# Kernel tuning notes

Measured on AMD Instinct MI355X. Metric: run time of the kernel, lower is better.

The kernel has to match this reference:

```python
import jax, jax.numpy as jnp
import numpy as np

B = 16384
D1 = 256
D2 = 256
D_FF = 1024
N_BINS = 16
TAIL = 3.0
MIN_VAL = 1e-3
MIN_TOTAL = N_BINS * MIN_VAL
TAIL_CONST = float(np.log(np.exp(1.0 - MIN_VAL) - 1.0))
D_OUT = (3 * N_BINS - 1) * D2  # 12032


def setup_inputs() -> dict:
    key = jax.random.key(0)
    ks = jax.random.split(key, 8)
    s = lambda fan: 1.0 / np.sqrt(fan)
    return {
        'x1': jax.random.normal(ks[0], (B, D1), jnp.float32),
        'x2': jax.random.normal(ks[1], (B, D2), jnp.float32),
        'W0': jax.random.normal(ks[2], (D1, D_FF), jnp.float32) * s(D1),
        'b0': jnp.zeros((D_FF,), jnp.float32),
        'W1': jax.random.normal(ks[3], (D_FF, D_FF), jnp.float32) * s(D_FF),
        'b1': jnp.zeros((D_FF,), jnp.float32),
        'W2': jax.random.normal(ks[4], (D_FF, D_OUT), jnp.float32) * s(D_FF),
        'b2': jnp.zeros((D_OUT,), jnp.float32),
    }


def _rqs_forward(x, wu, hu, du):
    # x: [B, D2]; wu, hu: [B, D2, N_BINS]; du: [B, D2, N_BINS-1]
    widths = MIN_VAL + (1.0 - MIN_TOTAL) * jax.nn.softmax(wu, axis=-1)
    heights = MIN_VAL + (1.0 - MIN_TOTAL) * jax.nn.softmax(hu, axis=-1)
    cw = jnp.cumsum(widths, axis=-1)
    cw = jnp.concatenate([jnp.zeros_like(cw[..., :1]), cw], axis=-1)
    cw = 2.0 * TAIL * cw - TAIL  # x bin edges in [-TAIL, TAIL], [B,D2,N_BINS+1]
    ch = jnp.cumsum(heights, axis=-1)
    ch = jnp.concatenate([jnp.zeros_like(ch[..., :1]), ch], axis=-1)
    ch = 2.0 * TAIL * ch - TAIL  # y bin edges
    w = cw[..., 1:] - cw[..., :-1]
    h = ch[..., 1:] - ch[..., :-1]
    # boundary derivatives padded so softplus(TAIL_CONST)+MIN_VAL == 1 (linear tails)
    pad = jnp.full_like(du[..., :1], TAIL_CONST)
    d = MIN_VAL + jax.nn.softplus(jnp.concatenate([pad, du, pad], axis=-1))  # [B,D2,N_BINS+1]
    inside = (x > -TAIL) & (x < TAIL)
    xc = jnp.clip(x, -TAIL, TAIL)
    # data-dependent bin search against interior edges
    idx = jnp.sum((xc[..., None] >= cw[..., 1:-1]).astype(jnp.int32), axis=-1)  # [B,D2]
    take = lambda a: jnp.take_along_axis(a, idx[..., None], axis=-1)[..., 0]
    xk = take(cw[..., :-1]); yk = take(ch[..., :-1])
    wk = take(w); hk = take(h)
    dk = take(d[..., :-1]); dk1 = take(d[..., 1:])
    sk = hk / wk
    theta = (xc - xk) / wk
    t1m = theta * (1.0 - theta)
    denom = sk + (dk + dk1 - 2.0 * sk) * t1m
    y = yk + hk * (sk * theta * theta + dk * t1m) / denom
    deriv = sk * sk * (dk1 * theta * theta + 2.0 * sk * t1m + dk * (1.0 - theta) ** 2) / (denom * denom)
    y = jnp.where(inside, y, x)            # identity tails
    logdet = jnp.where(inside, jnp.log(deriv), 0.0)
    return y, jnp.sum(logdet, axis=-1)     # [B,D2], [B]


def reference(x1, x2, W0, b0, W1, b1, W2, b2):
    # conditioner MLP: x1 -> spline parameters
    hdn = jax.nn.relu(x1 @ W0 + b0)
    hdn = jax.nn.relu(hdn @ W1 + b1)
    p = (hdn @ W2 + b2).reshape(-1, D2, 3 * N_BINS - 1)
    wu = p[..., :N_BINS]
    hu = p[..., N_BINS:2 * N_BINS]
    du = p[..., 2 * N_BINS:]
    y2, logdet = _rqs_forward(x2, wu, hu, du)
    return y2, logdet
```

## Files before the change

kernel.cpp:

```cpp
#include <hip/hip_runtime.h>
#include <math.h>

using u16 = unsigned short;
using bf16x8 = __attribute__((ext_vector_type(8))) short;
using f32x4  = __attribute__((ext_vector_type(4))) float;

#define DEV static __device__ __forceinline__

DEV u16 f2bf(float f) {
  union { float f; unsigned u; } v; v.f = f;
  unsigned u = v.u + 0x7fffu + ((v.u >> 16) & 1u);
  return (u16)(u >> 16);
}

DEV void gload16(const void* g, void* l) {
  __builtin_amdgcn_global_load_lds(
      (const __attribute__((address_space(1))) void*)g,
      (__attribute__((address_space(3))) void*)l, 16, 0, 0);
}

__global__ void k_conv_bf16(const float* __restrict__ in, u16* __restrict__ out, int n) {
  int i = blockIdx.x * 256 + threadIdx.x;
  if (i < n) out[i] = f2bf(in[i]);
}

__global__ void k_transconv(const float* __restrict__ in, u16* __restrict__ out,
                            int K, int Nin, int Nout, int pack) {
  __shared__ float t[32][33];
  int kb = blockIdx.x * 32, nb = blockIdx.y * 32;
  int tx = threadIdx.x & 31, ty = threadIdx.x >> 5;
  #pragma unroll
  for (int i = 0; i < 4; ++i) {
    int k = kb + ty + i * 8;
    int no = nb + tx;
    float v = 0.f;
    if (k < K && no < Nout) {
      if (pack) {
        int r = no % 48;
        if (r < 47) v = in[(size_t)k * Nin + (no / 48) * 47 + r];
      } else {
        v = in[(size_t)k * Nin + no];
      }
    }
    t[ty + i * 8][tx] = v;
  }
  __syncthreads();
  #pragma unroll
  for (int i = 0; i < 4; ++i) {
    int no = nb + ty + i * 8;
    int k = kb + tx;
    if (no < Nout && k < K) out[(size_t)no * K + k] = f2bf(t[tx][ty + i * 8]);
  }
}

__global__ __launch_bounds__(256)
void k_gemm_relu(const u16* __restrict__ A, const u16* __restrict__ Bt,
                 const float* __restrict__ bias, u16* __restrict__ C,
                 int N, int K) {
  constexpr int BM = 128, BN = 128, BK = 32;
  __shared__ __align__(16) u16 lds[(BM + BN) * BK];
  int tid = threadIdx.x, w = tid >> 6, lane = tid & 63;
  int bn = blockIdx.x, bm = blockIdx.y;
  int brow = bm * BM, bcol = bn * BN;
  int wm = w >> 1, wn = w & 1;
  int fr = lane & 15, fg = lane >> 4;
  f32x4 acc[4][4];
  #pragma unroll
  for (int i = 0; i < 4; ++i)
    #pragma unroll
    for (int j = 0; j < 4; ++j) acc[i][j] = (f32x4){0.f, 0.f, 0.f, 0.f};

  constexpr int ACH = BM * BK / 8;
  constexpr int CALLS = (BM + BN) * BK / 8 / 64;

  for (int kt = 0; kt < K; kt += BK) {
    for (int j = 0; j * 4 + w < CALLS; ++j) {
      int cb = (j * 4 + w) * 64;
      int c = cb + lane;
      const u16* g;
      if (c < ACH) {
        int row = c >> 2, c8 = c & 3;
        g = A + (size_t)(brow + row) * K + kt + c8 * 8;
      } else {
        int b = c - ACH;
        int nn = b >> 2, c8 = b & 3;
        g = Bt + (size_t)(bcol + nn) * K + kt + c8 * 8;
      }
      gload16(g, &lds[cb * 8]);
    }
    asm volatile("s_waitcnt vmcnt(0)" ::: "memory");
    __syncthreads();

    const u16* Al = lds;
    const u16* Bl = lds + BM * BK;
    bf16x8 af[4], bfr[4];
    #pragma unroll
    for (int mi = 0; mi < 4; ++mi)
      af[mi] = *(const bf16x8*)&Al[(wm * 64 + mi * 16 + fr) * BK + fg * 8];
    #pragma unroll
    for (int ni = 0; ni < 4; ++ni)
      bfr[ni] = *(const bf16x8*)&Bl[(wn * 64 + ni * 16 + fr) * BK + fg * 8];
    #pragma unroll
    for (int mi = 0; mi < 4; ++mi)
      #pragma unroll
      for (int ni = 0; ni < 4; ++ni)
        acc[mi][ni] = __builtin_amdgcn_mfma_f32_16x16x32_bf16(af[mi], bfr[ni], acc[mi][ni], 0, 0, 0);
    __syncthreads();
  }

  #pragma unroll
  for (int ni = 0; ni < 4; ++ni) {
    int col = bcol + wn * 64 + ni * 16 + fr;
    float bb = bias[col];
    #pragma unroll
    for (int mi = 0; mi < 4; ++mi) {
      #pragma unroll
      for (int q = 0; q < 4; ++q) {
        int row = brow + wm * 64 + mi * 16 + fg * 4 + q;
        float vv = acc[mi][ni][q] + bb;
        C[(size_t)row * N + col] = f2bf(vv > 0.f ? vv : 0.f);
      }
    }
  }
}

__global__ __launch_bounds__(256, 2)
void k_gemm3_fused(const u16* __restrict__ A, const u16* __restrict__ Bt,
                   const float* __restrict__ b2, const float* __restrict__ x2,
                   float* __restrict__ y2, float* __restrict__ ldpart) {
  extern __shared__ char smem[];
  const int tid = threadIdx.x, w = tid >> 6, lane = tid & 63;
  const int wm = w >> 1, wn = w & 1;
  const int fr = lane & 15, fg = lane >> 4;

  const int bid = blockIdx.x;
  const int bm = bid >> 6;
  const int bn = ((bid & 7) << 3) | ((bid >> 3) & 7);
  const int brow = bm * 128;

  const int csrc = (tid & 3) ^ ((tid >> 3) & 3);
  const u16* gA0 = A + (size_t)(brow + (tid >> 2)) * 1024 + csrc * 8;
  const u16* gB0 = Bt + (size_t)(bn * 192 + (tid >> 2)) * 1024 + csrc * 8;

#define STAGE(t1, sb) {                                               \
    const size_t ko_ = (size_t)(t1) * 32;                             \
    char* p_ = smem + (sb) + tid * 16;                                \
    gload16(gA0 + ko_, p_);                                           \
    gload16(gA0 + 65536 + ko_, p_ + 4096);                            \
    gload16(gB0 + ko_, p_ + 8192);                                    \
    gload16(gB0 + 65536 + ko_, p_ + 12288);                           \
    gload16(gB0 + 131072 + ko_, p_ + 16384); }

  const int sc = ((fg ^ ((fr >> 1) & 3)) << 4);

  f32x4 acc[4][6];
  #pragma unroll
  for (int m = 0; m < 4; ++m)
    #pragma unroll
    for (int n = 0; n < 6; ++n) acc[m][n] = (f32x4){0.f, 0.f, 0.f, 0.f};

#define COMPUTE(sb) {                                                 \
    const char* Ab_ = smem + (sb);                                    \
    const char* Bb_ = Ab_ + 8192;                                     \
    bf16x8 b_[6];                                                     \
    _Pragma("unroll")                                                 \
    for (int n_ = 0; n_ < 6; ++n_)                                    \
      b_[n_] = *(const bf16x8*)(Bb_ + (wn * 96 + n_ * 16 + fr) * 64 + sc); \
    __builtin_amdgcn_s_setprio(1);                                    \
    _Pragma("unroll")                                                 \
    for (int m_ = 0; m_ < 4; ++m_) {                                  \
      bf16x8 a_ = *(const bf16x8*)(Ab_ + (wm * 64 + m_ * 16 + fr) * 64 + sc); \
      _Pragma("unroll")                                               \
      for (int n_ = 0; n_ < 6; ++n_)                                  \
        acc[m_][n_] = __builtin_amdgcn_mfma_f32_16x16x32_bf16(a_, b_[n_], acc[m_][n_], 0, 0, 0); \
    }                                                                 \
    __builtin_amdgcn_s_setprio(0); }

#define VMW(n) { asm volatile("s_waitcnt vmcnt(" #n ")" ::: "memory"); \
                 __builtin_amdgcn_sched_barrier(0); }
#define RBAR() { __builtin_amdgcn_s_barrier(); __builtin_amdgcn_sched_barrier(0); }

  STAGE(0, 0); STAGE(1, 20480);
  VMW(5);
  RBAR();

  for (int j = 0; j < 10; ++j) {
    STAGE(3 * j + 2, 40960); COMPUTE(0);     VMW(5); RBAR();
    STAGE(3 * j + 3, 0);     COMPUTE(20480); VMW(5); RBAR();
    STAGE(3 * j + 4, 20480); COMPUTE(40960); VMW(5); RBAR();
  }
  COMPUTE(0); VMW(0); RBAR();
  COMPUTE(20480);
  __syncthreads();

  float* ldacc = (float*)(smem + 50176);
  float* fl = (float*)smem;
  #pragma unroll
  for (int rh = 0; rh < 2; ++rh) {
    if (wm == rh) {
      #pragma unroll
      for (int m = 0; m < 4; ++m)
        #pragma unroll
        for (int n = 0; n < 6; ++n) {
          const int g = wn * 2 + (n >= 3 ? 1 : 0);
          const int ci = (n % 3) * 16 + fr;
          #pragma unroll
          for (int q = 0; q < 4; ++q)
            fl[g * 3136 + (m * 16 + fg * 4 + q) * 49 + ci] = acc[m][n][q];
        }
    }
    __syncthreads();
    {
      const int g = tid >> 6, r = tid & 63;
      const float* pr = fl + g * 3136 + r * 49;
      const int grow = brow + rh * 64 + r;
      const int d2 = bn * 4 + g;
      const float* bb = b2 + (size_t)d2 * 47;

      float wv[16], hv[16];
      #pragma unroll
      for (int j = 0; j < 16; ++j) wv[j] = pr[j] + bb[j];
      #pragma unroll
      for (int j = 0; j < 16; ++j) hv[j] = pr[16 + j] + bb[16 + j];

      float x = x2[(size_t)grow * 256 + d2];
      float xc = fminf(fmaxf(x, -3.f), 3.f);

      float mw = wv[0];
      #pragma unroll
      for (int j = 1; j < 16; ++j) mw = fmaxf(mw, wv[j]);
      float sw = 0.f;
      #pragma unroll
      for (int j = 0; j < 16; ++j) { wv[j] = __expf(wv[j] - mw); sw += wv[j]; }
      float scw = 0.984f / sw;

      float mh = hv[0];
      #pragma unroll
      for (int j = 1; j < 16; ++j) mh = fmaxf(mh, hv[j]);
      float sh = 0.f;
      #pragma unroll
      for (int j = 0; j < 16; ++j) { hv[j] = __expf(hv[j] - mh); sh += hv[j]; }
      float sch = 0.984f / sh;

      int idx = 0;
      float xk = -3.f, cum = 0.f;
      #pragma unroll
      for (int i = 1; i <= 15; ++i) {
        cum += 0.001f + wv[i - 1] * scw;
        float cwi = 6.f * cum - 3.f;
        if (xc >= cwi) { idx = i; xk = cwi; }
      }
      float yk = -3.f, cumh = 0.f;
      #pragma unroll
      for (int i = 1; i <= 15; ++i) {
        cumh += 0.001f + hv[i - 1] * sch;
        float chi = 6.f * cumh - 3.f;
        if (i == idx) yk = chi;
      }
      float wk = 1.f, hk = 1.f;
      #pragma unroll
      for (int i = 0; i < 16; ++i) {
        if (i == idx) {
          wk = 6.f * (0.001f + wv[i] * scw);
          hk = 6.f * (0.001f + hv[i] * sch);
        }
      }
      float dk = 1.f, dk1 = 1.f;
      #pragma unroll
      for (int i = 1; i <= 15; ++i) {
        float u = pr[32 + i - 1] + bb[32 + i - 1];
        float e = __expf(u);
        float dd = 0.001f + (u > 15.f ? u : log1pf(e));
        if (i == idx) dk = dd;
        if (i == idx + 1) dk1 = dd;
      }

      float sk = hk / wk;
      float th = (xc - xk) / wk;
      float om = 1.f - th;
      float t1m = th * om;
      float den = sk + (dk + dk1 - 2.f * sk) * t1m;
      float y = yk + hk * (sk * th * th + dk * t1m) / den;
      float deriv = sk * sk * (dk1 * th * th + 2.f * sk * t1m + dk * om * om) / (den * den);
      bool inside = (x > -3.f) && (x < 3.f);
      float yout = inside ? y : x;
      float ld = inside ? __logf(deriv) : 0.f;

      y2[(size_t)grow * 256 + d2] = yout;
      ldacc[(rh * 64 + r) * 4 + g] = ld;
    }
    __syncthreads();
  }

  if (tid < 128) {
    float s = ldacc[tid * 4] + ldacc[tid * 4 + 1] + ldacc[tid * 4 + 2] + ldacc[tid * 4 + 3];
    ldpart[(size_t)bn * 16384 + brow + tid] = s;
  }
}

__global__ void k_reduce_ld(const float* __restrict__ part, float* __restrict__ out) {
  int r = blockIdx.x * 256 + threadIdx.x;
  float s = 0.f;
  for (int j = 0; j < 64; ++j) s += part[(size_t)j * 16384 + r];
  out[r] = s;
}

extern "C" void kernel_launch(void* const* d_in, const int* in_sizes, int n_in,
                              void* d_out, int out_size, void* d_ws, size_t ws_size,
                              hipStream_t stream) {
  const float* x1 = (const float*)d_in[0];
  const float* x2 = (const float*)d_in[1];
  const float* W0 = (const float*)d_in[2];
  const float* b0 = (const float*)d_in[3];
  const float* W1 = (const float*)d_in[4];
  const float* b1 = (const float*)d_in[5];
  const float* W2 = (const float*)d_in[6];
  const float* b2 = (const float*)d_in[7];
  float* y2 = (float*)d_out;
  float* logdet = y2 + (size_t)16384 * 256;

  char* ws = (char*)d_ws;
  u16* W2t = (u16*)ws;
  u16* W0t = (u16*)(ws + 25165824);
  u16* W1t = (u16*)(ws + 25165824 + 524288);
  u16* x1b = (u16*)(ws + 27787264);
  float* ldp = (float*)(ws + 27787264);
  u16* h1  = (u16*)(ws + 36175872);
  u16* h2  = (u16*)(ws + 69730304);

  hipFuncSetAttribute((const void*)k_gemm3_fused,
                      hipFuncAttributeMaxDynamicSharedMemorySize, 61440);

  k_conv_bf16<<<16384, 256, 0, stream>>>(x1, x1b, 16384 * 256);
  k_transconv<<<dim3(8, 32), 256, 0, stream>>>(W0, W0t, 256, 1024, 1024, 0);
  k_transconv<<<dim3(32, 32), 256, 0, stream>>>(W1, W1t, 1024, 1024, 1024, 0);
  k_transconv<<<dim3(32, 384), 256, 0, stream>>>(W2, W2t, 1024, 12032, 12288, 1);

  k_gemm_relu<<<dim3(8, 128), 256, 0, stream>>>(x1b, W0t, b0, h1, 1024, 256);
  k_gemm_relu<<<dim3(8, 128), 256, 0, stream>>>(h1, W1t, b1, h2, 1024, 1024);
  k_gemm3_fused<<<8192, 256, 61440, stream>>>(h2, W2t, b2, x2, y2, ldp);
  k_reduce_ld<<<64, 256, 0, stream>>>(ldp, logdet);
}
```

Measured before the change: 708.6 us.

## Pre-pack GEMM3 operands into tile-contiguous swizzled layout for contiguous loads

The second hidden GEMM and the W2 transpose-convert kernel now write their outputs in a blocked layout. Each 128-row (or 192-row) by 32-k tile is stored contiguously with the LDS XOR swizzle already applied. The fused GEMM3 then streams each stage as fully contiguous 16-byte chunks, with no strided per-row addressing. The aim is better global load coalescing and fewer TLB/row misses, at the cost of scattered 2-byte writes in the producer epilogues.

New measurement: 725.6 us. 1.02x slower.

```diff
diff --git a/kernel.cpp b/kernel.cpp
--- a/kernel.cpp
+++ b/kernel.cpp
@@ -49,14 +49,24 @@
   for (int i = 0; i < 4; ++i) {
     int no = nb + ty + i * 8;
     int k = kb + tx;
-    if (no < Nout && k < K) out[(size_t)no * K + k] = f2bf(t[tx][ty + i * 8]);
+    if (no < Nout && k < K) {
+      float v = t[tx][ty + i * 8];
+      if (pack) {
+        int r_ = no % 192, bn_ = no / 192;
+        int t_ = k >> 5, c_ = k & 31;
+        out[(((size_t)bn_ * 32 + t_) * 192 + r_) * 32
+            + (((c_ >> 3) ^ ((r_ >> 1) & 3)) << 3) + (c_ & 7)] = f2bf(v);
+      } else {
+        out[(size_t)no * K + k] = f2bf(v);
+      }
+    }
   }
 }
 
 __global__ __launch_bounds__(256)
 void k_gemm_relu(const u16* __restrict__ A, const u16* __restrict__ Bt,
                  const float* __restrict__ bias, u16* __restrict__ C,
-                 int N, int K) {
+                 int N, int K, int pack) {
   constexpr int BM = 128, BN = 128, BK = 32;
   __shared__ __align__(16) u16 lds[(BM + BN) * BK];
   int tid = threadIdx.x, w = tid >> 6, lane = tid & 63;
@@ -118,14 +128,21 @@
       for (int q = 0; q < 4; ++q) {
         int row = brow + wm * 64 + mi * 16 + fg * 4 + q;
         float vv = acc[mi][ni][q] + bb;
-        C[(size_t)row * N + col] = f2bf(vv > 0.f ? vv : 0.f);
+        u16 ov = f2bf(vv > 0.f ? vv : 0.f);
+        if (pack) {
+          int t_ = col >> 5, c_ = col & 31, r_ = row & 127;
+          C[(((size_t)(row >> 7) * 32 + t_) * 128 + r_) * 32
+            + (((c_ >> 3) ^ ((r_ >> 1) & 3)) << 3) + (c_ & 7)] = ov;
+        } else {
+          C[(size_t)row * N + col] = ov;
+        }
       }
     }
   }
 }
 
 __global__ __launch_bounds__(256, 2)
-void k_gemm3_fused(const u16* __restrict__ A, const u16* __restrict__ Bt,
+void k_gemm3_fused(const u16* __restrict__ Apack, const u16* __restrict__ Bpack,
                    const float* __restrict__ b2, const float* __restrict__ x2,
                    float* __restrict__ y2, float* __restrict__ ldpart) {
   extern __shared__ char smem[];
@@ -138,18 +155,18 @@
   const int bn = ((bid & 7) << 3) | ((bid >> 3) & 7);
   const int brow = bm * 128;
 
-  const int csrc = (tid & 3) ^ ((tid >> 3) & 3);
-  const u16* gA0 = A + (size_t)(brow + (tid >> 2)) * 1024 + csrc * 8;
-  const u16* gB0 = Bt + (size_t)(bn * 192 + (tid >> 2)) * 1024 + csrc * 8;
+  const u16* gA0 = Apack + (size_t)bm * 131072 + tid * 8;
+  const u16* gB0 = Bpack + (size_t)bn * 196608 + tid * 8;
 
 #define STAGE(t1, sb) {                                               \
-    const size_t ko_ = (size_t)(t1) * 32;                             \
+    const u16* pa_ = gA0 + (size_t)(t1) * 4096;                       \
+    const u16* pb_ = gB0 + (size_t)(t1) * 6144;                       \
     char* p_ = smem + (sb) + tid * 16;                                \
-    gload16(gA0 + ko_, p_);                                           \
-    gload16(gA0 + 65536 + ko_, p_ + 4096);                            \
-    gload16(gB0 + ko_, p_ + 8192);                                    \
-    gload16(gB0 + 65536 + ko_, p_ + 12288);                           \
-    gload16(gB0 + 131072 + ko_, p_ + 16384); }
+    gload16(pa_, p_);                                                 \
+    gload16(pa_ + 2048, p_ + 4096);                                   \
+    gload16(pb_, p_ + 8192);                                          \
+    gload16(pb_ + 2048, p_ + 12288);                                  \
+    gload16(pb_ + 4096, p_ + 16384); }
 
   const int sc = ((fg ^ ((fr >> 1) & 3)) << 4);
 
@@ -320,13 +337,13 @@
   float* logdet = y2 + (size_t)16384 * 256;
 
   char* ws = (char*)d_ws;
-  u16* W2t = (u16*)ws;
+  u16* W2p = (u16*)ws;
   u16* W0t = (u16*)(ws + 25165824);
   u16* W1t = (u16*)(ws + 25165824 + 524288);
   u16* x1b = (u16*)(ws + 27787264);
   float* ldp = (float*)(ws + 27787264);
   u16* h1  = (u16*)(ws + 36175872);
-  u16* h2  = (u16*)(ws + 69730304);
+  u16* h2p = (u16*)(ws + 69730304);
 
   hipFuncSetAttribute((const void*)k_gemm3_fused,
                       hipFuncAttributeMaxDynamicSharedMemorySize, 61440);
@@ -334,10 +351,10 @@
   k_conv_bf16<<<16384, 256, 0, stream>>>(x1, x1b, 16384 * 256);
   k_transconv<<<dim3(8, 32), 256, 0, stream>>>(W0, W0t, 256, 1024, 1024, 0);
   k_transconv<<<dim3(32, 32), 256, 0, stream>>>(W1, W1t, 1024, 1024, 1024, 0);
-  k_transconv<<<dim3(32, 384), 256, 0, stream>>>(W2, W2t, 1024, 12032, 12288, 1);
-
-  k_gemm_relu<<<dim3(8, 128), 256, 0, stream>>>(x1b, W0t, b0, h1, 1024, 256);
-  k_gemm_relu<<<dim3(8, 128), 256, 0, stream>>>(h1, W1t, b1, h2, 1024, 1024);
-  k_gemm3_fused<<<8192, 256, 61440, stream>>>(h2, W2t, b2, x2, y2, ldp);
+  k_transconv<<<dim3(32, 384), 256, 0, stream>>>(W2, W2p, 1024, 12032, 12288, 1);
+
+  k_gemm_relu<<<dim3(8, 128), 256, 0, stream>>>(x1b, W0t, b0, h1, 1024, 256, 0);
+  k_gemm_relu<<<dim3(8, 128), 256, 0, stream>>>(h1, W1t, b1, h2p, 1024, 1024, 1);
+  k_gemm3_fused<<<8192, 256, 61440, stream>>>(h2p, W2p, b2, x2, y2, ldp);
   k_reduce_ld<<<64, 256, 0, stream>>>(ldp, logdet);
 }
```
